# Optimization experiments

Hardware: AMD Instinct MI355X
Metric: run time of the kernel (lower is better)

## Reference

```python
import jax, jax.numpy as jnp
import numpy as np

S1, S2, S3 = 2, 16, 1  # hardcoded layer sizes from __init__


def _lstm_cell(x, h, c, w_ih, w_hh, b_ih, b_hh):
    # torch.nn.LSTMCell gate order: i, f, g, o
    gates = x @ w_ih.T + b_ih + h @ w_hh.T + b_hh
    i, f, g, o = jnp.split(gates, 4, axis=-1)
    i = jax.nn.sigmoid(i)
    f = jax.nn.sigmoid(f)
    g = jnp.tanh(g)
    o = jax.nn.sigmoid(o)
    c_new = f * c + i * g
    h_new = o * jnp.tanh(c_new)
    return h_new, c_new


def setup_inputs() -> dict:
    key = jax.random.key(0)
    ks = jax.random.split(key, 16)
    B, T = 16384, 2048
    x = jax.random.normal(ks[0], (B, T * S1), dtype=jnp.float32)

    def u(k, shape, fan):
        bound = 1.0 / np.sqrt(fan)
        return jax.random.uniform(k, shape, jnp.float32, -bound, bound)

    return {
        "x": x,
        # lstm1: LSTMCell(2, 2)
        "w_ih1": u(ks[1], (4 * S1, S1), S1), "w_hh1": u(ks[2], (4 * S1, S1), S1),
        "b_ih1": u(ks[3], (4 * S1,), S1),   "b_hh1": u(ks[4], (4 * S1,), S1),
        # lstm2: LSTMCell(2, 16)
        "w_ih2": u(ks[5], (4 * S2, S1), S2), "w_hh2": u(ks[6], (4 * S2, S2), S2),
        "b_ih2": u(ks[7], (4 * S2,), S2),   "b_hh2": u(ks[8], (4 * S2,), S2),
        # lstm3: LSTMCell(16, 1)
        "w_ih3": u(ks[9], (4 * S3, S2), S3), "w_hh3": u(ks[10], (4 * S3, S3), S3),
        "b_ih3": u(ks[11], (4 * S3,), S3),  "b_hh3": u(ks[12], (4 * S3,), S3),
        # linear: Linear(1, 1)
        "w_lin": u(ks[13], (S3, S3), S3), "b_lin": u(ks[14], (S3,), S3),
    }


def reference(x, w_ih1, w_hh1, b_ih1, b_hh1,
              w_ih2, w_hh2, b_ih2, b_hh2,
              w_ih3, w_hh3, b_ih3, b_hh3,
              w_lin, b_lin):
    B = x.shape[0]
    T = x.shape[1] // S1
    # [B, T*2] -> [T, B, 2] (time-major for scan)
    xt = x.reshape(B, T, S1).transpose(1, 0, 2)

    h1 = jnp.zeros((B, S1), x.dtype); c1 = jnp.zeros((B, S1), x.dtype)
    h2 = jnp.zeros((B, S2), x.dtype); c2 = jnp.zeros((B, S2), x.dtype)
    h3 = jnp.zeros((B, S3), x.dtype); c3 = jnp.zeros((B, S3), x.dtype)

    def step(carry, x_t):
        h1, c1, h2, c2, h3, c3 = carry
        h1, c1 = _lstm_cell(x_t, h1, c1, w_ih1, w_hh1, b_ih1, b_hh1)
        h2, c2 = _lstm_cell(h1, h2, c2, w_ih2, w_hh2, b_ih2, b_hh2)
        h3, c3 = _lstm_cell(h2, h3, c3, w_ih3, w_hh3, b_ih3, b_hh3)
        out = h3 @ w_lin.T + b_lin  # [B, 1]
        return (h1, c1, h2, c2, h3, c3), out

    _, ys = jax.lax.scan(step, (h1, c1, h2, c2, h3, c3), xt)
    # ys: [T, B, 1] -> cat along dim=1 of per-step [B,1] outputs -> [B, T]
    return ys[:, :, 0].T
```

## Files before the change

kernel.cpp:

```cpp
#include <hip/hip_runtime.h>

typedef _Float16 f16x8 __attribute__((ext_vector_type(8)));
typedef float    f32x4 __attribute__((ext_vector_type(4)));
typedef unsigned u32x4 __attribute__((ext_vector_type(4)));

#define DEV __device__ __forceinline__

DEV float fexp2(float x){ return __builtin_amdgcn_exp2f(x); }
DEV float frcp (float x){ return __builtin_amdgcn_rcpf(x); }
DEV float sigm(float x){ return frcp(1.0f + fexp2(x * -1.44269504088896341f)); }

DEV float shx(float v, int m){ return __shfl_xor(v, m, 64); }

DEV unsigned pkrne(float a, float b){
  unsigned short ha = __builtin_bit_cast(unsigned short, (_Float16)a);
  unsigned short hb = __builtin_bit_cast(unsigned short, (_Float16)b);
  return (unsigned)ha | ((unsigned)hb << 16);
}

__global__ __launch_bounds__(256, 1)
void lstm3_kernel(const float* __restrict__ x,
                  const float* __restrict__ w_ih1, const float* __restrict__ w_hh1,
                  const float* __restrict__ b_ih1, const float* __restrict__ b_hh1,
                  const float* __restrict__ w_ih2, const float* __restrict__ w_hh2,
                  const float* __restrict__ b_ih2, const float* __restrict__ b_hh2,
                  const float* __restrict__ w_ih3, const float* __restrict__ w_hh3,
                  const float* __restrict__ b_ih3, const float* __restrict__ b_hh3,
                  const float* __restrict__ w_lin, const float* __restrict__ b_lin,
                  float* __restrict__ out, int T)
{
  const int tid = threadIdx.x;
  const int l   = tid & 63;
  const int n   = l & 15;
  const int g   = l >> 4;
  const int wv  = tid >> 6;
  const int seq = 16 * (blockIdx.x * 4 + wv) + n;

  const int rA = g, rB = 4 + g;
  const float scB = (g < 2) ? 2.0f : 1.0f;
  const float m1  = (g < 2) ? 2.0f : 1.0f;
  const float a1  = (g < 2) ? -1.0f : 0.0f;
  const float w1ax = w_ih1[2*rA],      w1ay = w_ih1[2*rA+1];
  const float w1ah0 = w_hh1[2*rA],     w1ah1 = w_hh1[2*rA+1];
  const float bbA  = b_ih1[rA] + b_hh1[rA];
  const float w1bx = w_ih1[2*rB]*scB,  w1by = w_ih1[2*rB+1]*scB;
  const float w1bh0 = w_hh1[2*rB]*scB, w1bh1 = w_hh1[2*rB+1]*scB;
  const float bbB  = (b_ih1[rB] + b_hh1[rB]) * scB;

  f16x8 af[4];
  f16x8 a2f[4];
  f32x4 cb[4];
  #pragma unroll
  for (int t = 0; t < 4; ++t){
    const float sc = (t == 2) ? 2.0f : 1.0f;
    #pragma unroll
    for (int e = 0; e < 8; ++e){
      float v = 0.0f;
      if (e < 4) v = w_hh2[(16*t + n)*16 + (4*g + e)];
      af[t][e] = (_Float16)(v * sc);
      float v2 = 0.0f;
      if (g == 0 && e < 2) v2 = w_ih2[(16*t + n)*2 + e];
      a2f[t][e] = (_Float16)(v2 * sc);
    }
    #pragma unroll
    for (int j = 0; j < 4; ++j){
      const int r = 16*t + 4*g + j;
      cb[t][j] = (b_ih2[r] + b_hh2[r]) * sc;
    }
  }

  f16x8 a3f;
  #pragma unroll
  for (int e = 0; e < 8; ++e){
    float v = 0.0f;
    if ((n & 3) == 0 && e < 4){
      const int r = n >> 2;
      v = w_ih3[16*r + 4*g + e] * ((r == 2) ? 2.0f : 1.0f);
    }
    a3f[e] = (_Float16)v;
  }
  const float sc3 = (g == 2) ? 2.0f : 1.0f;
  const float m3  = (g == 2) ? 2.0f : 1.0f;
  const float a3  = (g == 2) ? -1.0f : 0.0f;
  const float wh3own = w_hh3[g] * sc3;
  const float bb3own = (b_ih3[g] + b_hh3[g]) * sc3;
  f32x4 c3v; c3v[0] = bb3own; c3v[1] = 0.f; c3v[2] = 0.f; c3v[3] = 0.f;
  const float wl = w_lin[0], bl = b_lin[0];

  float c1 = 0.f, c3 = 0.f;
  float c2[4] = {0.f, 0.f, 0.f, 0.f};
  float h1a_all = 0.f, h1b_all = 0.f, h3_all = 0.f;
  unsigned pAu = 0u, pBu = 0u;

  const float* xrow = x + (size_t)seq * (size_t)(2*T);
  float*       orow = out + (size_t)seq * (size_t)T;

  float4 pa = *(const float4*)(xrow);
  float4 pb = *(const float4*)(xrow + 4);

  float o0 = 0.f, o1 = 0.f, o2 = 0.f, o3 = 0.f;

  const int NCH = T / 4;
  for (int ch = 0; ch < NCH; ++ch){
    const float4 ca = pa, cbv = pb;
    const int no = (ch + 1 < NCH) ? (ch + 1) * 8 : 0;
    pa = *(const float4*)(xrow + no);
    pb = *(const float4*)(xrow + no + 4);

    const bool cap = (g == (ch & 3));

    #pragma unroll
    for (int s = 0; s < 4; ++s){
      const float x0 = (s==0)?ca.x:(s==1)?ca.z:(s==2)?cbv.x:cbv.z;
      const float x1 = (s==0)?ca.y:(s==1)?ca.w:(s==2)?cbv.y:cbv.w;

      u32x4 bu; bu[0] = pAu; bu[1] = pBu; bu[2] = 0u; bu[3] = 0u;
      const f16x8 bv = __builtin_bit_cast(f16x8, bu);
      f32x4 d0 = __builtin_amdgcn_mfma_f32_16x16x32_f16(af[0], bv, cb[0], 0, 0, 0);
      f32x4 d1 = __builtin_amdgcn_mfma_f32_16x16x32_f16(af[1], bv, cb[1], 0, 0, 0);
      f32x4 d2 = __builtin_amdgcn_mfma_f32_16x16x32_f16(af[2], bv, cb[2], 0, 0, 0);
      f32x4 d3 = __builtin_amdgcn_mfma_f32_16x16x32_f16(af[3], bv, cb[3], 0, 0, 0);

      const float gA = fmaf(w1ax, x0, fmaf(w1ay, x1,
                       fmaf(w1ah0, h1a_all, fmaf(w1ah1, h1b_all, bbA))));
      const float gB = fmaf(w1bx, x0, fmaf(w1by, x1,
                       fmaf(w1bh0, h1a_all, fmaf(w1bh1, h1b_all, bbB))));
      const float zA = sigm(gA);
      const float zB = fmaf(sigm(gB), m1, a1);
      const float ig1 = zA * zB;
      const float fm = shx(zA, 32);
      c1 = fmaf(fm, c1, ig1);
      const float th1 = fmaf(2.f, sigm(c1 + c1), -1.f);
      const float om = shx(zB, 32);
      const float h1v = om * th1;
      const float t16 = shx(h1v, 16);
      const unsigned h1p = pkrne(h1v, t16);
      u32x4 b2u; b2u[0] = (g == 0) ? h1p : 0u; b2u[1] = 0u; b2u[2] = 0u; b2u[3] = 0u;
      const f16x8 b2v = __builtin_bit_cast(f16x8, b2u);
      const float a_c = (g & 1) ? t16 : h1v;
      const float b_c = (g & 1) ? h1v : t16;
      const float a32 = shx(a_c, 32);
      const float b32 = shx(b_c, 32);
      h1a_all = (g & 2) ? a32 : a_c;
      h1b_all = (g & 2) ? b32 : b_c;

      d0 = __builtin_amdgcn_mfma_f32_16x16x32_f16(a2f[0], b2v, d0, 0, 0, 0);
      d1 = __builtin_amdgcn_mfma_f32_16x16x32_f16(a2f[1], b2v, d1, 0, 0, 0);
      d2 = __builtin_amdgcn_mfma_f32_16x16x32_f16(a2f[2], b2v, d2, 0, 0, 0);
      d3 = __builtin_amdgcn_mfma_f32_16x16x32_f16(a2f[3], b2v, d3, 0, 0, 0);

      float h2l[4];
      #pragma unroll
      for (int j = 0; j < 4; ++j){
        const float ii = sigm(d0[j]);
        const float ff = sigm(d1[j]);
        const float gg = fmaf(2.f, sigm(d2[j]), -1.f);
        const float oo = sigm(d3[j]);
        c2[j] = fmaf(ff, c2[j], ii * gg);
        const float th = fmaf(2.f, sigm(c2[j] + c2[j]), -1.f);
        h2l[j] = oo * th;
      }
      pAu = pkrne(h2l[0], h2l[1]);
      pBu = pkrne(h2l[2], h2l[3]);

      u32x4 b3u; b3u[0] = pAu; b3u[1] = pBu; b3u[2] = 0u; b3u[3] = 0u;
      const f16x8 b3v = __builtin_bit_cast(f16x8, b3u);
      const f32x4 d3v = __builtin_amdgcn_mfma_f32_16x16x32_f16(a3f, b3v, c3v, 0, 0, 0);
      const float P = fmaf(wh3own, h3_all, d3v[0]);
      const float z  = fmaf(sigm(P), m3, a3);
      const float gvv = shx(z, 32);
      const float ig3 = z * gvv;
      const float fv = shx(z, 16);
      c3 = fmaf(fv, c3, ig3);
      const float th3 = fmaf(2.f, sigm(c3 + c3), -1.f);
      const float ov3 = shx(gvv, 16);
      const float h3v = ov3 * th3;
      const float u16 = shx(h3v, 16);
      const float selh = (g & 1) ? u16 : h3v;
      const float u32v = shx(selh, 32);
      h3_all = (g & 2) ? u32v : selh;
      const float yv = fmaf(wl, h3_all, bl);

      if      (s == 0) o0 = cap ? yv : o0;
      else if (s == 1) o1 = cap ? yv : o1;
      else if (s == 2) o2 = cap ? yv : o2;
      else             o3 = cap ? yv : o3;
    }

    if ((ch & 3) == 3){
      float4 o4; o4.x = o0; o4.y = o1; o4.z = o2; o4.w = o3;
      *(float4*)(orow + (ch >> 2) * 16 + 4 * g) = o4;
    }
  }
}

extern "C" void kernel_launch(void* const* d_in, const int* in_sizes, int n_in,
                              void* d_out, int out_size, void* d_ws, size_t ws_size,
                              hipStream_t stream)
{
  const float* x     = (const float*)d_in[0];
  const float* w_ih1 = (const float*)d_in[1];
  const float* w_hh1 = (const float*)d_in[2];
  const float* b_ih1 = (const float*)d_in[3];
  const float* b_hh1 = (const float*)d_in[4];
  const float* w_ih2 = (const float*)d_in[5];
  const float* w_hh2 = (const float*)d_in[6];
  const float* b_ih2 = (const float*)d_in[7];
  const float* b_hh2 = (const float*)d_in[8];
  const float* w_ih3 = (const float*)d_in[9];
  const float* w_hh3 = (const float*)d_in[10];
  const float* b_ih3 = (const float*)d_in[11];
  const float* b_hh3 = (const float*)d_in[12];
  const float* w_lin = (const float*)d_in[13];
  const float* b_lin = (const float*)d_in[14];
  float* out = (float*)d_out;

  const int T = 2048;
  const int B = in_sizes[0] / (2 * T);
  const int waves   = B / 16;
  const int blocks  = waves / 4;

  lstm3_kernel<<<blocks, 256, 0, stream>>>(
      x, w_ih1, w_hh1, b_ih1, b_hh1,
      w_ih2, w_hh2, b_ih2, b_hh2,
      w_ih3, w_hh3, b_ih3, b_hh3,
      w_lin, b_lin, out, T);
}
```

Baseline: 1.209 ms.

## Prescale gate weights by log2e, hoist recurrent MFMA, compute layer-3 gates redundantly

Gate weights and biases are pre-multiplied by -log2(e) (or -2log2(e) for tanh gates), so each sigmoid skips one multiply. The layer-2 recurrent MFMA (W_hh2·h2) is moved to the end of the previous step, right after h2 is produced, so it overlaps with layer-3 work and is off the critical path of the next step's layer-1 computation. Layer 3 now has every lane compute all four gates from a broadcast MFMA result instead of splitting gates across lane groups. This removes several cross-lane shuffles per step at the cost of extra transcendental work.

```diff
diff --git a/kernel.cpp b/kernel.cpp
--- a/kernel.cpp
+++ b/kernel.cpp
@@ -8,7 +8,9 @@
 
 DEV float fexp2(float x){ return __builtin_amdgcn_exp2f(x); }
 DEV float frcp (float x){ return __builtin_amdgcn_rcpf(x); }
-DEV float sigm(float x){ return frcp(1.0f + fexp2(x * -1.44269504088896341f)); }
+
+DEV float sgm(float p){ return frcp(1.0f + fexp2(p)); }
+DEV float tnc(float c){ return fmaf(2.f, sgm(c * -2.88539008177792682f), -1.f); }
 
 DEV float shx(float v, int m){ return __shfl_xor(v, m, 64); }
 
@@ -17,6 +19,9 @@
   unsigned short hb = __builtin_bit_cast(unsigned short, (_Float16)b);
   return (unsigned)ha | ((unsigned)hb << 16);
 }
+
+#define L2E_N  (-1.44269504088896341f)
+#define L2E2_N (-2.88539008177792682f)
 
 __global__ __launch_bounds__(256, 1)
 void lstm3_kernel(const float* __restrict__ x,
@@ -37,22 +42,23 @@
   const int seq = 16 * (blockIdx.x * 4 + wv) + n;
 
   const int rA = g, rB = 4 + g;
-  const float scB = (g < 2) ? 2.0f : 1.0f;
+  const float sAq = L2E_N;
+  const float sBq = (g < 2) ? L2E2_N : L2E_N;
   const float m1  = (g < 2) ? 2.0f : 1.0f;
   const float a1  = (g < 2) ? -1.0f : 0.0f;
-  const float w1ax = w_ih1[2*rA],      w1ay = w_ih1[2*rA+1];
-  const float w1ah0 = w_hh1[2*rA],     w1ah1 = w_hh1[2*rA+1];
-  const float bbA  = b_ih1[rA] + b_hh1[rA];
-  const float w1bx = w_ih1[2*rB]*scB,  w1by = w_ih1[2*rB+1]*scB;
-  const float w1bh0 = w_hh1[2*rB]*scB, w1bh1 = w_hh1[2*rB+1]*scB;
-  const float bbB  = (b_ih1[rB] + b_hh1[rB]) * scB;
+  const float w1ax = w_ih1[2*rA]*sAq,  w1ay = w_ih1[2*rA+1]*sAq;
+  const float w1ah0 = w_hh1[2*rA]*sAq, w1ah1 = w_hh1[2*rA+1]*sAq;
+  const float bbA  = (b_ih1[rA] + b_hh1[rA]) * sAq;
+  const float w1bx = w_ih1[2*rB]*sBq,  w1by = w_ih1[2*rB+1]*sBq;
+  const float w1bh0 = w_hh1[2*rB]*sBq, w1bh1 = w_hh1[2*rB+1]*sBq;
+  const float bbB  = (b_ih1[rB] + b_hh1[rB]) * sBq;
 
   f16x8 af[4];
   f16x8 a2f[4];
   f32x4 cb[4];
   #pragma unroll
   for (int t = 0; t < 4; ++t){
-    const float sc = (t == 2) ? 2.0f : 1.0f;
+    const float sc = (t == 2) ? L2E2_N : L2E_N;
     #pragma unroll
     for (int e = 0; e < 8; ++e){
       float v = 0.0f;
@@ -69,27 +75,30 @@
     }
   }
 
+  const float s3n = ((n & 3) == 2) ? L2E2_N : L2E_N;
   f16x8 a3f;
   #pragma unroll
   for (int e = 0; e < 8; ++e){
     float v = 0.0f;
-    if ((n & 3) == 0 && e < 4){
-      const int r = n >> 2;
-      v = w_ih3[16*r + 4*g + e] * ((r == 2) ? 2.0f : 1.0f);
-    }
+    if (e < 4) v = w_ih3[16*(n & 3) + 4*g + e] * s3n;
     a3f[e] = (_Float16)v;
   }
-  const float sc3 = (g == 2) ? 2.0f : 1.0f;
-  const float m3  = (g == 2) ? 2.0f : 1.0f;
-  const float a3  = (g == 2) ? -1.0f : 0.0f;
-  const float wh3own = w_hh3[g] * sc3;
-  const float bb3own = (b_ih3[g] + b_hh3[g]) * sc3;
-  f32x4 c3v; c3v[0] = bb3own; c3v[1] = 0.f; c3v[2] = 0.f; c3v[3] = 0.f;
+  f32x4 c3v;
+  float wh3s0, wh3s1, wh3s2, wh3s3;
+  {
+    const float s0 = L2E_N, s1 = L2E_N, s2 = L2E2_N, s3_ = L2E_N;
+    c3v[0] = (b_ih3[0] + b_hh3[0]) * s0;
+    c3v[1] = (b_ih3[1] + b_hh3[1]) * s1;
+    c3v[2] = (b_ih3[2] + b_hh3[2]) * s2;
+    c3v[3] = (b_ih3[3] + b_hh3[3]) * s3_;
+    wh3s0 = w_hh3[0] * s0; wh3s1 = w_hh3[1] * s1;
+    wh3s2 = w_hh3[2] * s2; wh3s3 = w_hh3[3] * s3_;
+  }
   const float wl = w_lin[0], bl = b_lin[0];
 
   float c1 = 0.f, c3 = 0.f;
   float c2[4] = {0.f, 0.f, 0.f, 0.f};
-  float h1a_all = 0.f, h1b_all = 0.f, h3_all = 0.f;
+  float h1a_all = 0.f, h1b_all = 0.f, h3 = 0.f;
   unsigned pAu = 0u, pBu = 0u;
 
   const float* xrow = x + (size_t)seq * (size_t)(2*T);
@@ -99,6 +108,16 @@
   float4 pb = *(const float4*)(xrow + 4);
 
   float o0 = 0.f, o1 = 0.f, o2 = 0.f, o3 = 0.f;
+
+  f32x4 dp0, dp1, dp2, dp3;
+  {
+    u32x4 bu; bu[0] = 0u; bu[1] = 0u; bu[2] = 0u; bu[3] = 0u;
+    const f16x8 bv = __builtin_bit_cast(f16x8, bu);
+    dp0 = __builtin_amdgcn_mfma_f32_16x16x32_f16(af[0], bv, cb[0], 0, 0, 0);
+    dp1 = __builtin_amdgcn_mfma_f32_16x16x32_f16(af[1], bv, cb[1], 0, 0, 0);
+    dp2 = __builtin_amdgcn_mfma_f32_16x16x32_f16(af[2], bv, cb[2], 0, 0, 0);
+    dp3 = __builtin_amdgcn_mfma_f32_16x16x32_f16(af[3], bv, cb[3], 0, 0, 0);
+  }
 
   const int NCH = T / 4;
   for (int ch = 0; ch < NCH; ++ch){
@@ -114,23 +133,16 @@
       const float x0 = (s==0)?ca.x:(s==1)?ca.z:(s==2)?cbv.x:cbv.z;
       const float x1 = (s==0)?ca.y:(s==1)?ca.w:(s==2)?cbv.y:cbv.w;
 
-      u32x4 bu; bu[0] = pAu; bu[1] = pBu; bu[2] = 0u; bu[3] = 0u;
-      const f16x8 bv = __builtin_bit_cast(f16x8, bu);
-      f32x4 d0 = __builtin_amdgcn_mfma_f32_16x16x32_f16(af[0], bv, cb[0], 0, 0, 0);
-      f32x4 d1 = __builtin_amdgcn_mfma_f32_16x16x32_f16(af[1], bv, cb[1], 0, 0, 0);
-      f32x4 d2 = __builtin_amdgcn_mfma_f32_16x16x32_f16(af[2], bv, cb[2], 0, 0, 0);
-      f32x4 d3 = __builtin_amdgcn_mfma_f32_16x16x32_f16(af[3], bv, cb[3], 0, 0, 0);
-
       const float gA = fmaf(w1ax, x0, fmaf(w1ay, x1,
                        fmaf(w1ah0, h1a_all, fmaf(w1ah1, h1b_all, bbA))));
       const float gB = fmaf(w1bx, x0, fmaf(w1by, x1,
                        fmaf(w1bh0, h1a_all, fmaf(w1bh1, h1b_all, bbB))));
-      const float zA = sigm(gA);
-      const float zB = fmaf(sigm(gB), m1, a1);
+      const float zA = sgm(gA);
+      const float zB = fmaf(sgm(gB), m1, a1);
       const float ig1 = zA * zB;
       const float fm = shx(zA, 32);
       c1 = fmaf(fm, c1, ig1);
-      const float th1 = fmaf(2.f, sigm(c1 + c1), -1.f);
+      const float th1 = tnc(c1);
       const float om = shx(zB, 32);
       const float h1v = om * th1;
       const float t16 = shx(h1v, 16);
@@ -144,42 +156,43 @@
       h1a_all = (g & 2) ? a32 : a_c;
       h1b_all = (g & 2) ? b32 : b_c;
 
-      d0 = __builtin_amdgcn_mfma_f32_16x16x32_f16(a2f[0], b2v, d0, 0, 0, 0);
-      d1 = __builtin_amdgcn_mfma_f32_16x16x32_f16(a2f[1], b2v, d1, 0, 0, 0);
-      d2 = __builtin_amdgcn_mfma_f32_16x16x32_f16(a2f[2], b2v, d2, 0, 0, 0);
-      d3 = __builtin_amdgcn_mfma_f32_16x16x32_f16(a2f[3], b2v, d3, 0, 0, 0);
+      const f32x4 d0 = __builtin_amdgcn_mfma_f32_16x16x32_f16(a2f[0], b2v, dp0, 0, 0, 0);
+      const f32x4 d1 = __builtin_amdgcn_mfma_f32_16x16x32_f16(a2f[1], b2v, dp1, 0, 0, 0);
+      const f32x4 d2 = __builtin_amdgcn_mfma_f32_16x16x32_f16(a2f[2], b2v, dp2, 0, 0, 0);
+      const f32x4 d3 = __builtin_amdgcn_mfma_f32_16x16x32_f16(a2f[3], b2v, dp3, 0, 0, 0);
 
       float h2l[4];
       #pragma unroll
       for (int j = 0; j < 4; ++j){
-        const float ii = sigm(d0[j]);
-        const float ff = sigm(d1[j]);
-        const float gg = fmaf(2.f, sigm(d2[j]), -1.f);
-        const float oo = sigm(d3[j]);
+        const float ii = sgm(d0[j]);
+        const float ff = sgm(d1[j]);
+        const float gg = fmaf(2.f, sgm(d2[j]), -1.f);
+        const float oo = sgm(d3[j]);
         c2[j] = fmaf(ff, c2[j], ii * gg);
-        const float th = fmaf(2.f, sigm(c2[j] + c2[j]), -1.f);
-        h2l[j] = oo * th;
+        h2l[j] = oo * tnc(c2[j]);
       }
       pAu = pkrne(h2l[0], h2l[1]);
       pBu = pkrne(h2l[2], h2l[3]);
 
-      u32x4 b3u; b3u[0] = pAu; b3u[1] = pBu; b3u[2] = 0u; b3u[3] = 0u;
-      const f16x8 b3v = __builtin_bit_cast(f16x8, b3u);
-      const f32x4 d3v = __builtin_amdgcn_mfma_f32_16x16x32_f16(a3f, b3v, c3v, 0, 0, 0);
-      const float P = fmaf(wh3own, h3_all, d3v[0]);
-      const float z  = fmaf(sigm(P), m3, a3);
-      const float gvv = shx(z, 32);
-      const float ig3 = z * gvv;
-      const float fv = shx(z, 16);
-      c3 = fmaf(fv, c3, ig3);
-      const float th3 = fmaf(2.f, sigm(c3 + c3), -1.f);
-      const float ov3 = shx(gvv, 16);
-      const float h3v = ov3 * th3;
-      const float u16 = shx(h3v, 16);
-      const float selh = (g & 1) ? u16 : h3v;
-      const float u32v = shx(selh, 32);
-      h3_all = (g & 2) ? u32v : selh;
-      const float yv = fmaf(wl, h3_all, bl);
+      u32x4 bu; bu[0] = pAu; bu[1] = pBu; bu[2] = 0u; bu[3] = 0u;
+      const f16x8 bv = __builtin_bit_cast(f16x8, bu);
+      dp0 = __builtin_amdgcn_mfma_f32_16x16x32_f16(af[0], bv, cb[0], 0, 0, 0);
+      dp1 = __builtin_amdgcn_mfma_f32_16x16x32_f16(af[1], bv, cb[1], 0, 0, 0);
+      dp2 = __builtin_amdgcn_mfma_f32_16x16x32_f16(af[2], bv, cb[2], 0, 0, 0);
+      dp3 = __builtin_amdgcn_mfma_f32_16x16x32_f16(af[3], bv, cb[3], 0, 0, 0);
+
+      const f32x4 d3v = __builtin_amdgcn_mfma_f32_16x16x32_f16(a3f, bv, c3v, 0, 0, 0);
+      const float p_i = fmaf(wh3s0, h3, d3v[0]);
+      const float p_f = fmaf(wh3s1, h3, d3v[1]);
+      const float p_g = fmaf(wh3s2, h3, d3v[2]);
+      const float p_o = fmaf(wh3s3, h3, d3v[3]);
+      const float i3 = sgm(p_i);
+      const float f3 = sgm(p_f);
+      const float g3 = fmaf(2.f, sgm(p_g), -1.f);
+      const float q3 = sgm(p_o);
+      c3 = fmaf(f3, c3, i3 * g3);
+      h3 = q3 * tnc(c3);
+      const float yv = fmaf(wl, h3, bl);
 
       if      (s == 0) o0 = cap ? yv : o0;
       else if (s == 1) o1 = cap ? yv : o1;
```

New measurement: 1.060 ms. 1.14x faster.
